# Optimization experiments

Hardware: AMD Instinct MI355X
Metric: run time of the kernel (lower is better)

Reference implementation:

```python
import jax, jax.numpy as jnp
import numpy as np

N_FFT = 1024
HOP = 256
WIN = N_FFT  # win_length = n_fft in VocosISTFTHead
PAD = (WIN - HOP) // 2  # 384, 'same' padding trim
CLAMP_MAX = 100.0


def _hann_periodic(n):
    # matches torch.hann_window(n, periodic=True)
    return 0.5 * (1.0 - jnp.cos(2.0 * jnp.pi * jnp.arange(n, dtype=jnp.float32) / n))


def setup_inputs() -> dict:
    key = jax.random.key(0)
    k1, k2, k3 = jax.random.split(key, 3)
    B, T, H = 16, 2048, 512
    hidden_states = jax.random.normal(k1, (B, T, H), dtype=jnp.float32)
    # out_proj: Linear(hidden_dim, n_fft+2); scaled so exp(magnitude) stays sane
    W = jax.random.normal(k2, (N_FFT + 2, H), dtype=jnp.float32) * 0.02
    b = jax.random.normal(k3, (N_FFT + 2,), dtype=jnp.float32) * 0.02
    window = _hann_periodic(WIN)
    return {"hidden_states": hidden_states, "W": W, "b": b, "window": window}


def reference(hidden_states, W, b, window):
    B, T, _ = hidden_states.shape
    # linear projection -> [B, T, n_fft+2] -> transpose -> [B, n_fft+2, T]
    spec = (hidden_states @ W.T + b).transpose(0, 2, 1)
    half = (N_FFT + 2) // 2  # n_fft//2 + 1 = 513 freq bins
    magnitude = jnp.minimum(jnp.exp(spec[:, :half]), CLAMP_MAX)
    phase = spec[:, half:]
    coeffs = magnitude * (jnp.cos(phase) + 1j * jnp.sin(phase))  # [B, F, T] complex
    # inverse rfft along freq axis, norm='backward' (default) -> [B, n_fft, T]
    frames = jnp.fft.irfft(coeffs, n=N_FFT, axis=1)
    frames = frames * window[None, :, None]
    L = (T - 1) * HOP + WIN
    idx = (jnp.arange(T)[:, None] * HOP + jnp.arange(WIN)[None, :]).reshape(-1)
    frames_flat = frames.transpose(0, 2, 1).reshape(B, -1)
    audio = jnp.zeros((B, L), frames.dtype).at[:, idx].add(frames_flat)
    # NOLA normalization: overlap-added squared window
    wsq = jnp.broadcast_to(window ** 2, (T, WIN)).reshape(-1)
    norm = jnp.zeros((L,), window.dtype).at[idx].add(wsq)
    return audio[:, PAD:-PAD] / norm[PAD:-PAD]
```

## Files before the change

kernel.cpp:

```cpp
#include <hip/hip_runtime.h>
#include <hip/hip_fp16.h>
#include <math.h>
#include <stdint.h>


#define FRAMES  32768
#define TWO_PI  6.283185307179586f

typedef unsigned short ushort_t;
typedef __attribute__((ext_vector_type(8))) _Float16 f16x8;
typedef __attribute__((ext_vector_type(4))) float f32x4;

#define GLDS(gp, lp) __builtin_amdgcn_global_load_lds( \
    (const __attribute__((address_space(1))) void*)(gp), \
    (__attribute__((address_space(3))) void*)(lp), 16, 0, 0)

__device__ __forceinline__ float2 f2(float x, float y){ return make_float2(x,y); }
__device__ __forceinline__ float2 cadd(float2 a, float2 b){ return f2(a.x+b.x, a.y+b.y); }
__device__ __forceinline__ float2 csub(float2 a, float2 b){ return f2(a.x-b.x, a.y-b.y); }
__device__ __forceinline__ float2 cmul(float2 a, float2 b){ return f2(a.x*b.x - a.y*b.y, a.x*b.y + a.y*b.x); }

__device__ __forceinline__ uint32_t pack2h(float a, float b) {
  const ushort_t ha = __half_as_ushort(__float2half_rn(a));
  const ushort_t hb = __half_as_ushort(__float2half_rn(b));
  return (uint32_t)ha | ((uint32_t)hb << 16);
}

__global__ __launch_bounds__(256) void convert_AB(
    const float* __restrict__ hs, const float* __restrict__ Wm,
    const float* __restrict__ bias, ushort_t* __restrict__ Af,
    ushort_t* __restrict__ Whi, __half* __restrict__ coeffs)
{
  const int bid = blockIdx.x;
  const int t = threadIdx.x;
  if (bid < 2048) {
    const int r = t >> 4, c = t & 15;
    const int m = bid * 16 + r;
    const float* src = hs + (size_t)m * 512 + c * 32;
    const float* wm  = Wm + (size_t)512  * 512 + c * 32;
    const float* wp  = Wm + (size_t)1025 * 512 + c * 32;

    float v[32];
    #pragma unroll
    for (int i = 0; i < 8; ++i) *(float4*)&v[i*4] = *(const float4*)(src + i*4);

    float dm = 0.f, dp = 0.f;
    #pragma unroll
    for (int i = 0; i < 8; ++i) {
      const float4 a  = *(const float4*)&v[i*4];
      const float4 m4 = *(const float4*)(wm + i*4);
      const float4 p4 = *(const float4*)(wp + i*4);
      dm = fmaf(a.x,m4.x, fmaf(a.y,m4.y, fmaf(a.z,m4.z, fmaf(a.w,m4.w, dm))));
      dp = fmaf(a.x,p4.x, fmaf(a.y,p4.y, fmaf(a.z,p4.z, fmaf(a.w,p4.w, dp))));
    }

    uint32_t hu[16];
    #pragma unroll
    for (int i = 0; i < 16; ++i) hu[i] = pack2h(v[2*i], v[2*i+1]);
    ushort_t* dh = Af + (size_t)m * 512 + c * 32;
    #pragma unroll
    for (int q = 0; q < 4; ++q)
      *(uint4*)(dh + q*8) = make_uint4(hu[4*q], hu[4*q+1], hu[4*q+2], hu[4*q+3]);

    #pragma unroll
    for (int off = 8; off; off >>= 1) {
      dm += __shfl_xor(dm, off, 16);
      dp += __shfl_xor(dp, off, 16);
    }
    if (c == 0) {
      const float sm = dm + bias[512], sp = dp + bias[1025];
      const float mag = fminf(__expf(sm), 100.0f);
      coeffs[(size_t)m * 1024 + 1] = __float2half_rn(mag * __cosf(sp));
    }
  } else {
    const int gid = (bid - 2048) * 256 + t;
    const int sd = gid & 3;
    const int r  = (gid >> 2) & 255;
    const int kt = (gid >> 10) & 15;
    const int yb = gid >> 14;
    const int srow = (r < 128) ? (yb*128 + r) : (513 + yb*128 + (r - 128));
    const float* src = Wm + (size_t)srow * 512 + kt*32 + sd*8;
    const float4 a = *(const float4*)src;
    const float4 b = *(const float4*)(src + 4);
    const uint4 o = make_uint4(pack2h(a.x,a.y), pack2h(a.z,a.w),
                               pack2h(b.x,b.y), pack2h(b.z,b.w));
    *(uint4*)(Whi + (size_t)gid * 8) = o;
  }
}

__global__ __launch_bounds__(512, 2) void gemm_mfma(
    const ushort_t* __restrict__ Af, const ushort_t* __restrict__ Whi,
    const float* __restrict__ bias, __half* __restrict__ coeffs)
{
  __shared__ ushort_t Ab[24576];

  const int tid = threadIdx.x;
  const int w = tid >> 6, l = tid & 63;
  const int wr = w >> 2, wc = w & 3;
  const int lc = l & 15, kg = l >> 4;

  const int bid = blockIdx.x;
  const int swz = (bid & 7) * 64 + (bid >> 3);
  const int mb = swz >> 2, yb = swz & 3;

  uint32_t pa_off[2], lofs[2];
  #pragma unroll
  for (int ch = 0; ch < 2; ++ch) {
    const int g = ch*512 + tid;
    const int r = g >> 2, sd = g & 3;
    lofs[ch] = r*32 + sd*8;
    const int sl = sd ^ ((r >> 1) & 3);
    pa_off[ch] = (uint32_t)(mb*256 + r)*512 + sl*8;
  }
  uint32_t pb_off[4];
  #pragma unroll
  for (int cf = 0; cf < 4; ++cf) {
    const int rB = ((cf < 2) ? 0 : 128) + wc*32 + (cf & 1)*16 + lc;
    pb_off[cf] = (uint32_t)yb*131072u + rB*32 + kg*8;
  }

  f32x4 acc[8][4];
  #pragma unroll
  for (int rf = 0; rf < 8; ++rf)
    #pragma unroll
    for (int cf = 0; cf < 4; ++cf)
      #pragma unroll
      for (int q = 0; q < 4; ++q) acc[rf][cf][q] = 0.f;

  const int asl = (kg ^ ((lc >> 1) & 3)) * 8;

  f16x8 p[4], q[4];

#define WAITV2 asm volatile("s_waitcnt vmcnt(2) lgkmcnt(0)" ::: "memory")
#define WAITV0 asm volatile("s_waitcnt vmcnt(0) lgkmcnt(0)" ::: "memory")
#define SB     __builtin_amdgcn_s_barrier()
#define SCH0   __builtin_amdgcn_sched_barrier(0)

#define DSREAD(DST, BASE, RF0) do {                                      \
    _Pragma("unroll")                                                    \
    for (int r4 = 0; r4 < 4; ++r4) {                                     \
      const int rr = wr*128 + ((RF0) + r4)*16 + lc;                      \
      DST[r4] = *(const f16x8*)(&Ab[(BASE) + rr*32 + asl]);              \
    }                                                                    \
  } while (0)

#define MFMA16(FA, RF0, RB) do {                                         \
    __builtin_amdgcn_s_setprio(1);                                       \
    _Pragma("unroll")                                                    \
    for (int r4 = 0; r4 < 4; ++r4)                                       \
      _Pragma("unroll")                                                  \
      for (int cf = 0; cf < 4; ++cf)                                     \
        acc[(RF0)+r4][cf] = __builtin_amdgcn_mfma_f32_16x16x32_f16(      \
            FA[r4], RB[cf], acc[(RF0)+r4][cf], 0, 0, 0);                 \
    __builtin_amdgcn_s_setprio(0);                                       \
  } while (0)

#define ITER(KT, RBC, RBN, LAST) do {                                    \
    if (LAST) { WAITV0; } else { WAITV2; }                               \
    SB;                                                                  \
               \
    DSREAD(q, aR, 4);                                                    \
    if ((KT) < 14) GLDS(Af + pa_off[0] + ((KT)+2)*32, &Ab[aW + lofs[0]]);\
    if ((KT) < 15) {                                                     \
      RBN[0] = *(const f16x8*)(Whi + pb_off[0] + ((KT)+1)*8192);         \
      RBN[1] = *(const f16x8*)(Whi + pb_off[1] + ((KT)+1)*8192);         \
    }                                                                    \
    SCH0;                                                                \
    MFMA16(p, 0, RBC);                                                   \
     \
    if ((KT) < 15) DSREAD(p, aN, 0);                                     \
    if ((KT) < 14) GLDS(Af + pa_off[1] + ((KT)+2)*32, &Ab[aW + lofs[1]]);\
    if ((KT) < 15) {                                                     \
      RBN[2] = *(const f16x8*)(Whi + pb_off[2] + ((KT)+1)*8192);         \
      RBN[3] = *(const f16x8*)(Whi + pb_off[3] + ((KT)+1)*8192);         \
    }                                                                    \
    SCH0;                                                                \
    MFMA16(q, 4, RBC);                                                   \
    { const unsigned t_ = aR; aR = aN; aN = aW; aW = t_; }               \
  } while (0)

  f16x8 rb0[4], rb1[4];
  GLDS(Af + pa_off[0], &Ab[lofs[0]]);
  GLDS(Af + pa_off[1], &Ab[lofs[1]]);
  GLDS(Af + pa_off[0] + 32, &Ab[8192 + lofs[0]]);
  GLDS(Af + pa_off[1] + 32, &Ab[8192 + lofs[1]]);
  SCH0;
  #pragma unroll
  for (int j = 0; j < 4; ++j) rb0[j] = *(const f16x8*)(Whi + pb_off[j]);
  SCH0;
  asm volatile("s_waitcnt vmcnt(6)" ::: "memory");
  SB;
  unsigned aR = 0, aN = 8192, aW = 16384;
  DSREAD(p, aR, 0);

  for (int k2 = 0; k2 < 8; ++k2) {
    ITER(2*k2,     rb0, rb1, false);
    ITER(2*k2 + 1, rb1, rb0, k2 == 7);
  }
#undef ITER
#undef DSREAD
#undef MFMA16

  const int pc0 = yb*128 + wc*32 + lc;
  const int pc1 = pc0 + 16;
  const float bm0 = bias[pc0], bp0 = bias[513 + pc0];
  const float bm1 = bias[pc1], bp1 = bias[513 + pc1];
  #pragma unroll
  for (int rf = 0; rf < 8; ++rf) {
    const int rbase = mb*256 + wr*128 + rf*16 + kg*4;
    #pragma unroll
    for (int qi = 0; qi < 4; ++qi) {
      __half* row = coeffs + (size_t)(rbase + qi) * 1024;
      {
        const float sm = acc[rf][0][qi] + bm0;
        const float sp = acc[rf][2][qi] + bp0;
        const float mag = fminf(__expf(sm), 100.0f);
        const float aa = mag * __cosf(sp);
        const float bb = mag * __sinf(sp);
        if (pc0 == 0) row[0] = __float2half_rn(aa);
        else *(__half2*)(row + 2*pc0) = __float22half2_rn(make_float2(aa, bb));
      }
      {
        const float sm = acc[rf][1][qi] + bm1;
        const float sp = acc[rf][3][qi] + bp1;
        const float mag = fminf(__expf(sm), 100.0f);
        const float aa = mag * __cosf(sp);
        const float bb = mag * __sinf(sp);
        *(__half2*)(row + 2*pc1) = __float22half2_rn(make_float2(aa, bb));
      }
    }
  }
}

#define PIDX(s) ((s) + ((s) >> 3))
#define WFENCE  __builtin_amdgcn_wave_barrier()

template<int NS>
__device__ __forceinline__ void stage_fft(const float2* in, float2* out, int l)
{
  float2 v[8];
  #pragma unroll
  for (int r = 0; r < 8; ++r) v[r] = in[PIDX(l + 64*r)];
  if (NS > 1) {
    const float ang = TWO_PI * (float)(l & (NS-1)) / (float)(NS * 8);
    float sn, cs; __sincosf(ang, &sn, &cs);
    const float2 wb = f2(cs, sn);
    float2 cur = wb;
    #pragma unroll
    for (int r = 1; r < 8; ++r) { v[r] = cmul(v[r], cur); cur = cmul(cur, wb); }
  }
  const float2 e0=v[0], e1=v[2], e2=v[4], e3=v[6];
  const float2 o0=v[1], o1=v[3], o2=v[5], o3=v[7];
  float2 a = cadd(e0,e2), b = csub(e0,e2), c = cadd(e1,e3), d = csub(e1,e3);
  const float2 E0 = cadd(a,c), E2 = csub(a,c);
  const float2 E1 = f2(b.x - d.y, b.y + d.x), E3 = f2(b.x + d.y, b.y - d.x);
  a = cadd(o0,o2); b = csub(o0,o2); c = cadd(o1,o3); d = csub(o1,o3);
  const float2 O0 = cadd(a,c), O2 = csub(a,c);
  const float2 O1 = f2(b.x - d.y, b.y + d.x), O3 = f2(b.x + d.y, b.y - d.x);
  const float r2 = 0.70710678118654752f;
  const float2 t0 = O0;
  const float2 t1 = f2(r2*(O1.x - O1.y),  r2*(O1.x + O1.y));
  const float2 t2 = f2(-O2.y, O2.x);
  const float2 t3 = f2(-r2*(O3.x + O3.y), r2*(O3.x - O3.y));
  float2 X[8];
  X[0]=cadd(E0,t0); X[4]=csub(E0,t0);
  X[1]=cadd(E1,t1); X[5]=csub(E1,t1);
  X[2]=cadd(E2,t2); X[6]=csub(E2,t2);
  X[3]=cadd(E3,t3); X[7]=csub(E3,t3);
  const int idxD = (l / NS) * (NS * 8) + (l & (NS-1));
  #pragma unroll
  for (int q = 0; q < 8; ++q) out[PIDX(idxD + q*NS)] = X[q];
}

__global__ __launch_bounds__(256) void fft_win(
    const __half* coeffs, __half* frames, const float* __restrict__ window)
{
  __shared__ float2 bA[4][576];
  __shared__ float2 bB[4][576];
  const int tid = threadIdx.x;
  const int w = tid >> 6, l = tid & 63;
  const size_t f = (size_t)blockIdx.x * 4 + w;
  const __half2* crow = (const __half2*)(coeffs + f * 1024);

  const float sc = 1.0f / 1024.0f;
  #pragma unroll
  for (int j = 0; j < 4; ++j) {
    const int k = 1 + l + 64*j;
    const float2 Ck = __half22float2(crow[k]);
    const float2 Cq = __half22float2(crow[512-k]);
    float sn, cs; __sincosf(TWO_PI * (1.0f/1024.0f) * (float)k, &sn, &cs);
    const float Ex = sc*(Ck.x + Cq.x), Ey = sc*(Ck.y - Cq.y);
    const float Dx = Ck.x - Cq.x,      Dy = Ck.y + Cq.y;
    const float Ox = sc*(cs*Dx - sn*Dy), Oy = sc*(cs*Dy + sn*Dx);
    bA[w][PIDX(k)]     = f2(Ex - Oy, Ey + Ox);
    bA[w][PIDX(512-k)] = f2(Ex + Oy, Ox - Ey);
  }
  if (l == 0) {
    const float2 dn = __half22float2(crow[0]);
    bA[w][PIDX(0)] = f2(sc*(dn.x + dn.y), sc*(dn.x - dn.y));
  }
  WFENCE;
  stage_fft<1 >(bA[w], bB[w], l);
  WFENCE;
  stage_fft<8 >(bB[w], bA[w], l);
  WFENCE;
  stage_fft<64>(bA[w], bB[w], l);
  WFENCE;

  __half2* frow = (__half2*)(frames + f * 1024);
  #pragma unroll
  for (int j = 0; j < 8; ++j) {
    const int m = l + 64*j;
    const float2 z  = bB[w][PIDX(m)];
    const float2 wv = *(const float2*)(window + 2*m);
    frow[m] = __float22half2_rn(make_float2(z.x * wv.x, z.y * wv.y));
  }
}

__global__ __launch_bounds__(256) void gather_out(
    const __half* __restrict__ frames, const float* __restrict__ window,
    float* __restrict__ out)
{
  const int idx = blockIdx.x * 256 + threadIdx.x;
  const int b  = idx >> 17;
  const int g  = idx & 131071;
  const int s  = g * 4 + 384;
  int tlo = (s - 768) >> 8; if (tlo < 0) tlo = 0;
  int thi = s >> 8;         if (thi > 2047) thi = 2047;
  float a0=0.f, a1=0.f, a2=0.f, a3=0.f;
  float n0=0.f, n1=0.f, n2=0.f, n3=0.f;
  const __half* fb = frames + (size_t)b * 2048 * 1024;
  for (int t = tlo; t <= thi; ++t) {
    const int n = s - (t << 8);
    const float4 wv = *(const float4*)(window + n);
    const uint2 fr = *(const uint2*)(fb + (size_t)t * 1024 + n);
    const float2 f01 = __half22float2(*(const __half2*)&fr.x);
    const float2 f23 = __half22float2(*(const __half2*)&fr.y);
    a0 += f01.x; a1 += f01.y; a2 += f23.x; a3 += f23.y;
    n0 = fmaf(wv.x, wv.x, n0); n1 = fmaf(wv.y, wv.y, n1);
    n2 = fmaf(wv.z, wv.z, n2); n3 = fmaf(wv.w, wv.w, n3);
  }
  *(float4*)(out + (size_t)idx * 4) = make_float4(a0/n0, a1/n1, a2/n2, a3/n3);
}

extern "C" void kernel_launch(void* const* d_in, const int* in_sizes, int n_in,
                              void* d_out, int out_size, void* d_ws, size_t ws_size,
                              hipStream_t stream)
{
  const float* hs     = (const float*)d_in[0];
  const float* Wm     = (const float*)d_in[1];
  const float* bias   = (const float*)d_in[2];
  const float* window = (const float*)d_in[3];

  char* base = (char*)d_ws;
  ushort_t* Af     = (ushort_t*)base;
  ushort_t* Whi    = (ushort_t*)(base + 33554432);
  __half*   frames = (__half*)base;
  __half*   coeffs = (__half*)(base + 67108864);

  convert_AB<<<2304, 256, 0, stream>>>(hs, Wm, bias, Af, Whi, coeffs);
  gemm_mfma<<<512,  512, 0, stream>>>(Af, Whi, bias, coeffs);
  fft_win<<<FRAMES / 4, 256, 0, stream>>>(coeffs, frames, window);
  gather_out<<<8192, 256, 0, stream>>>(frames, window, (float*)d_out);
}
```

Before: 134.2 us.

## Fuse inverse FFT, windowing and overlap-add into one kernel via shared memory

Merges the FFT+window kernel and the gather overlap-add kernel into a single kernel. Each block computes 12 overlapping frames (9 new plus 3 halo frames) into shared memory and produces 9 hops of output directly. This removes the global round-trip of the fp16 frames buffer and one kernel launch. The cost is 3/12 redundant FFT work for the halo frames. The last FFT stage also now writes windowed results straight to the shared frame tile.

New measurement: 145.3 us. +8.3%, slower.

```diff
diff --git a/kernel.cpp b/kernel.cpp
--- a/kernel.cpp
+++ b/kernel.cpp
@@ -6,6 +6,9 @@
 
 #define FRAMES  32768
 #define TWO_PI  6.283185307179586f
+#define FPB 12
+#define SPB 9
+#define BPB 228
 
 typedef unsigned short ushort_t;
 typedef __attribute__((ext_vector_type(8))) _Float16 f16x8;
@@ -158,7 +161,6 @@
 #define ITER(KT, RBC, RBN, LAST) do {                                    \
     if (LAST) { WAITV0; } else { WAITV2; }                               \
     SB;                                                                  \
-               \
     DSREAD(q, aR, 4);                                                    \
     if ((KT) < 14) GLDS(Af + pa_off[0] + ((KT)+2)*32, &Ab[aW + lofs[0]]);\
     if ((KT) < 15) {                                                     \
@@ -167,7 +169,6 @@
     }                                                                    \
     SCH0;                                                                \
     MFMA16(p, 0, RBC);                                                   \
-     \
     if ((KT) < 15) DSREAD(p, aN, 0);                                     \
     if ((KT) < 14) GLDS(Af + pa_off[1] + ((KT)+2)*32, &Ab[aW + lofs[1]]);\
     if ((KT) < 15) {                                                     \
@@ -272,75 +273,120 @@
   for (int q = 0; q < 8; ++q) out[PIDX(idxD + q*NS)] = X[q];
 }
 
-__global__ __launch_bounds__(256) void fft_win(
-    const __half* coeffs, __half* frames, const float* __restrict__ window)
+__device__ __forceinline__ void stage_last(const float2* in, __half* frout,
+                                           const float* __restrict__ window, int l)
+{
+  float2 v[8];
+  #pragma unroll
+  for (int r = 0; r < 8; ++r) v[r] = in[PIDX(l + 64*r)];
+  {
+    const float ang = TWO_PI * (float)l / 512.0f;
+    float sn, cs; __sincosf(ang, &sn, &cs);
+    const float2 wb = f2(cs, sn);
+    float2 cur = wb;
+    #pragma unroll
+    for (int r = 1; r < 8; ++r) { v[r] = cmul(v[r], cur); cur = cmul(cur, wb); }
+  }
+  const float2 e0=v[0], e1=v[2], e2=v[4], e3=v[6];
+  const float2 o0=v[1], o1=v[3], o2=v[5], o3=v[7];
+  float2 a = cadd(e0,e2), b = csub(e0,e2), c = cadd(e1,e3), d = csub(e1,e3);
+  const float2 E0 = cadd(a,c), E2 = csub(a,c);
+  const float2 E1 = f2(b.x - d.y, b.y + d.x), E3 = f2(b.x + d.y, b.y - d.x);
+  a = cadd(o0,o2); b = csub(o0,o2); c = cadd(o1,o3); d = csub(o1,o3);
+  const float2 O0 = cadd(a,c), O2 = csub(a,c);
+  const float2 O1 = f2(b.x - d.y, b.y + d.x), O3 = f2(b.x + d.y, b.y - d.x);
+  const float r2 = 0.70710678118654752f;
+  const float2 t0 = O0;
+  const float2 t1 = f2(r2*(O1.x - O1.y),  r2*(O1.x + O1.y));
+  const float2 t2 = f2(-O2.y, O2.x);
+  const float2 t3 = f2(-r2*(O3.x + O3.y), r2*(O3.x - O3.y));
+  float2 X[8];
+  X[0]=cadd(E0,t0); X[4]=csub(E0,t0);
+  X[1]=cadd(E1,t1); X[5]=csub(E1,t1);
+  X[2]=cadd(E2,t2); X[6]=csub(E2,t2);
+  X[3]=cadd(E3,t3); X[7]=csub(E3,t3);
+  #pragma unroll
+  for (int q = 0; q < 8; ++q) {
+    const int m = l + 64*q;
+    const float2 wv = *(const float2*)(window + 2*m);
+    *(__half2*)&frout[2*m] =
+        __float22half2_rn(make_float2(X[q].x * wv.x, X[q].y * wv.y));
+  }
+}
+
+__global__ __launch_bounds__(256) void fft_oa(
+    const __half* __restrict__ coeffs, const float* __restrict__ window,
+    float* __restrict__ out)
 {
   __shared__ float2 bA[4][576];
   __shared__ float2 bB[4][576];
+  __shared__ __half fr[FPB][1024];
+
   const int tid = threadIdx.x;
   const int w = tid >> 6, l = tid & 63;
-  const size_t f = (size_t)blockIdx.x * 4 + w;
-  const __half2* crow = (const __half2*)(coeffs + f * 1024);
-
+  const int bid = blockIdx.x;
+  const int b = bid / BPB, j = bid - b * BPB;
+  const int f0 = SPB * j - 3;
   const float sc = 1.0f / 1024.0f;
-  #pragma unroll
-  for (int j = 0; j < 4; ++j) {
-    const int k = 1 + l + 64*j;
-    const float2 Ck = __half22float2(crow[k]);
-    const float2 Cq = __half22float2(crow[512-k]);
-    float sn, cs; __sincosf(TWO_PI * (1.0f/1024.0f) * (float)k, &sn, &cs);
-    const float Ex = sc*(Ck.x + Cq.x), Ey = sc*(Ck.y - Cq.y);
-    const float Dx = Ck.x - Cq.x,      Dy = Ck.y + Cq.y;
-    const float Ox = sc*(cs*Dx - sn*Dy), Oy = sc*(cs*Dy + sn*Dx);
-    bA[w][PIDX(k)]     = f2(Ex - Oy, Ey + Ox);
-    bA[w][PIDX(512-k)] = f2(Ex + Oy, Ox - Ey);
-  }
-  if (l == 0) {
-    const float2 dn = __half22float2(crow[0]);
-    bA[w][PIDX(0)] = f2(sc*(dn.x + dn.y), sc*(dn.x - dn.y));
-  }
-  WFENCE;
-  stage_fft<1 >(bA[w], bB[w], l);
-  WFENCE;
-  stage_fft<8 >(bB[w], bA[w], l);
-  WFENCE;
-  stage_fft<64>(bA[w], bB[w], l);
-  WFENCE;
-
-  __half2* frow = (__half2*)(frames + f * 1024);
-  #pragma unroll
-  for (int j = 0; j < 8; ++j) {
-    const int m = l + 64*j;
-    const float2 z  = bB[w][PIDX(m)];
-    const float2 wv = *(const float2*)(window + 2*m);
-    frow[m] = __float22half2_rn(make_float2(z.x * wv.x, z.y * wv.y));
-  }
-}
-
-__global__ __launch_bounds__(256) void gather_out(
-    const __half* __restrict__ frames, const float* __restrict__ window,
-    float* __restrict__ out)
-{
-  const int idx = blockIdx.x * 256 + threadIdx.x;
-  const int b  = idx >> 17;
-  const int g  = idx & 131071;
-  const int s  = g * 4 + 384;
-  int tlo = (s - 768) >> 8; if (tlo < 0) tlo = 0;
-  int thi = s >> 8;         if (thi > 2047) thi = 2047;
-  float a0=0.f, a1=0.f, a2=0.f, a3=0.f;
-  float n0=0.f, n1=0.f, n2=0.f, n3=0.f;
-  const __half* fb = frames + (size_t)b * 2048 * 1024;
-  for (int t = tlo; t <= thi; ++t) {
-    const int n = s - (t << 8);
-    const float4 wv = *(const float4*)(window + n);
-    const uint2 fr = *(const uint2*)(fb + (size_t)t * 1024 + n);
-    const float2 f01 = __half22float2(*(const __half2*)&fr.x);
-    const float2 f23 = __half22float2(*(const __half2*)&fr.y);
-    a0 += f01.x; a1 += f01.y; a2 += f23.x; a3 += f23.y;
-    n0 = fmaf(wv.x, wv.x, n0); n1 = fmaf(wv.y, wv.y, n1);
-    n2 = fmaf(wv.z, wv.z, n2); n3 = fmaf(wv.w, wv.w, n3);
-  }
-  *(float4*)(out + (size_t)idx * 4) = make_float4(a0/n0, a1/n1, a2/n2, a3/n3);
+
+  for (int i = 0; i < 3; ++i) {
+    const int lf = 3*w + i;
+    const int f  = f0 + lf;
+    if (f < 0 || f > 2047) {
+      #pragma unroll
+      for (int jj = 0; jj < 8; ++jj)
+        *(__half2*)&fr[lf][2*(l + 64*jj)] = __half2();
+      continue;
+    }
+    const __half2* crow = (const __half2*)(coeffs + (size_t)(b*2048 + f) * 1024);
+    #pragma unroll
+    for (int jj = 0; jj < 4; ++jj) {
+      const int k = 1 + l + 64*jj;
+      const float2 Ck = __half22float2(crow[k]);
+      const float2 Cq = __half22float2(crow[512-k]);
+      float sn, cs; __sincosf(TWO_PI * (1.0f/1024.0f) * (float)k, &sn, &cs);
+      const float Ex = sc*(Ck.x + Cq.x), Ey = sc*(Ck.y - Cq.y);
+      const float Dx = Ck.x - Cq.x,      Dy = Ck.y + Cq.y;
+      const float Ox = sc*(cs*Dx - sn*Dy), Oy = sc*(cs*Dy + sn*Dx);
+      bA[w][PIDX(k)]     = f2(Ex - Oy, Ey + Ox);
+      bA[w][PIDX(512-k)] = f2(Ex + Oy, Ox - Ey);
+    }
+    if (l == 0) {
+      const float2 dn = __half22float2(crow[0]);
+      bA[w][PIDX(0)] = f2(sc*(dn.x + dn.y), sc*(dn.x - dn.y));
+    }
+    WFENCE;
+    stage_fft<1>(bA[w], bB[w], l);
+    WFENCE;
+    stage_fft<8>(bB[w], bA[w], l);
+    WFENCE;
+    stage_last(bA[w], fr[lf], window, l);
+    WFENCE;
+  }
+  __syncthreads();
+
+  float wsq[4];
+  #pragma unroll
+  for (int i = 0; i < 4; ++i) {
+    const float wv = window[tid + 256*i];
+    wsq[i] = wv * wv;
+  }
+  float* outb = out + (size_t)b * 524288;
+  #pragma unroll
+  for (int k = 0; k < SPB; ++k) {
+    const int t = SPB*j + k;
+    const int o = 256*t + tid - 384;
+    float acc = 0.f, nrm = 0.f;
+    #pragma unroll
+    for (int i = 0; i < 4; ++i) {
+      const int f = t - i;
+      if (f >= 0 && f <= 2047) {
+        acc += __half2float(fr[k + 3 - i][tid + 256*i]);
+        nrm += wsq[i];
+      }
+    }
+    if (o >= 0 && o < 524288) outb[o] = acc / nrm;
+  }
 }
 
 extern "C" void kernel_launch(void* const* d_in, const int* in_sizes, int n_in,
@@ -355,11 +401,9 @@
   char* base = (char*)d_ws;
   ushort_t* Af     = (ushort_t*)base;
   ushort_t* Whi    = (ushort_t*)(base + 33554432);
-  __half*   frames = (__half*)base;
   __half*   coeffs = (__half*)(base + 67108864);
 
   convert_AB<<<2304, 256, 0, stream>>>(hs, Wm, bias, Af, Whi, coeffs);
   gemm_mfma<<<512,  512, 0, stream>>>(Af, Whi, bias, coeffs);
-  fft_win<<<FRAMES / 4, 256, 0, stream>>>(coeffs, frames, window);
-  gather_out<<<8192, 256, 0, stream>>>(frames, window, (float*)d_out);
-}
+  fft_oa<<<16 * BPB, 256, 0, stream>>>(coeffs, window, (float*)d_out);
+}
```
